# Kernel optimization log

Measured on AMD Instinct MI355X. Metric: run time of the kernel, lower is better.

## Reference

```python
import jax, jax.numpy as jnp
import numpy as np

N = 200000   # nodes
E = 400000   # edges
G = 4096     # graphs in batch
F_IN = 77    # atom feature dim
D = 128      # dim_drug
L = 3        # layer_drug
BN_EPS = 1e-5


def setup_inputs() -> dict:
    key = jax.random.key(0)
    ks = jax.random.split(key, 16)
    inp = {}
    inp["x"] = jax.random.normal(ks[0], (N, F_IN), jnp.float32)
    inp["edge_index"] = jax.random.randint(ks[1], (2, E), 0, N, dtype=jnp.int64)
    inp["batch"] = jnp.sort(jax.random.randint(ks[2], (N,), 0, G, dtype=jnp.int64))
    dims = [F_IN, D, D]
    i = 3
    for l in range(L):
        din = dims[l]
        inp[f"w1_{l}"] = jax.random.normal(ks[i], (din, D), jnp.float32) / np.sqrt(din); i += 1
        inp[f"b1_{l}"] = jnp.zeros((D,), jnp.float32)
        inp[f"w2_{l}"] = jax.random.normal(ks[i], (D, D), jnp.float32) / np.sqrt(D); i += 1
        inp[f"b2_{l}"] = jnp.zeros((D,), jnp.float32)
        inp[f"gamma_{l}"] = jnp.ones((D,), jnp.float32)
        inp[f"beta_{l}"] = jnp.zeros((D,), jnp.float32)
    inp["w_emb"] = jax.random.normal(ks[i], (L * D, 256), jnp.float32) / np.sqrt(L * D)
    inp["b_emb"] = jnp.zeros((256,), jnp.float32)
    return inp


def _gin_bn_layer(h, src, dst, w1, b1, w2, b2, gamma, beta):
    # GINConv (eps=0): out_i = MLP(x_i + sum_{j->i} x_j)
    agg = jax.ops.segment_sum(h[src], dst, num_segments=N)  # scatter-add aggregation
    h = h + agg
    h = jax.nn.relu(h @ w1 + b1) @ w2 + b2                  # GIN MLP
    h = jax.nn.relu(h)                                       # outer F.relu
    mu = jnp.mean(h, axis=0)
    var = jnp.var(h, axis=0)                                  # biased var (training-mode BN)
    return (h - mu) * jax.lax.rsqrt(var + BN_EPS) * gamma + beta


def reference(x, edge_index, batch,
              w1_0, b1_0, w2_0, b2_0, gamma_0, beta_0,
              w1_1, b1_1, w2_1, b2_1, gamma_1, beta_1,
              w1_2, b1_2, w2_2, b2_2, gamma_2, beta_2,
              w_emb, b_emb):
    src, dst = edge_index[0], edge_index[1]
    layers = [(w1_0, b1_0, w2_0, b2_0, gamma_0, beta_0),
              (w1_1, b1_1, w2_1, b2_1, gamma_1, beta_1),
              (w1_2, b1_2, w2_2, b2_2, gamma_2, beta_2)]
    h = x
    outs = []
    for (w1, b1, w2, b2, g, b) in layers:
        h = _gin_bn_layer(h, src, dst, w1, b1, w2, b2, g, b)
        outs.append(h)
    node_rep = jnp.concatenate(outs, axis=1)                  # JK 'cat' -> [N, L*D]
    pooled = jax.ops.segment_max(node_rep, batch, num_segments=G)  # global_max_pool -> [G, L*D]
    # drug_emb: Linear -> ReLU -> Dropout (identity in eval)
    return jax.nn.relu(pooled @ w_emb + b_emb)
```

## Files before the change

kernel.cpp:

```cpp
#include <hip/hip_runtime.h>
#include <hip/hip_bf16.h>
#include <float.h>

#define NN 200000
#define NE 400000
#define NG 4096
#define FIN 77
#define DD 128
#define BN_EPS 1e-5f
#define NB_SCAN ((NN + 255) / 256)
#define NBLK (NN / 64)
#define WCAP 1024

#define XCONV_BLKS (NN * 12 / 256)
#define WCONV_BLKS 192
#define ZERO_WORDS16 50194
#define ZERO_BLKS ((ZERO_WORDS16 + 255) / 256)

typedef float f32x4 __attribute__((ext_vector_type(4)));
typedef short s16x8 __attribute__((ext_vector_type(8)));
typedef unsigned int u32x4 __attribute__((ext_vector_type(4)));

__device__ __forceinline__ unsigned short f2bf(float x) {
    unsigned b = __float_as_uint(x);
    unsigned r = (b + 0x7FFFu + ((b >> 16) & 1u)) >> 16;
    return (unsigned short)r;
}
__device__ __forceinline__ float bf2f(unsigned short u) {
    return __uint_as_float(((unsigned)u) << 16);
}

__device__ __forceinline__ int load_idx(const void* p, int is64, long long i) {
    return is64 ? (int)((const long long*)p)[i] : ((const int*)p)[i];
}

__global__ __launch_bounds__(256) void prep_kernel(
    const float* __restrict__ x, unsigned short* __restrict__ xb,
    const float* __restrict__ w10, const float* __restrict__ w20,
    const float* __restrict__ w11, const float* __restrict__ w21,
    const float* __restrict__ w12, const float* __restrict__ w22,
    unsigned short* __restrict__ wtb,
    unsigned int* __restrict__ zbase,
    const unsigned* __restrict__ eidx, const unsigned* __restrict__ batch,
    int* __restrict__ flags)
{
    int b = blockIdx.x;
    if (b < XCONV_BLKS) {
        int idx = b * 256 + threadIdx.x;
        int row = idx / 12, c8 = (idx % 12) * 8;
        union { s16x8 v; unsigned short u[8]; } pk;
#pragma unroll
        for (int j = 0; j < 8; j++) {
            int c = c8 + j;
            pk.u[j] = (c < FIN) ? f2bf(x[(long long)row * FIN + c]) : (unsigned short)0;
        }
        *(s16x8*)&xb[(long long)row * 96 + c8] = pk.v;
    } else if (b < XCONV_BLKS + WCONV_BLKS) {
        int bb = b - XCONV_BLKS;
        int l = bb >> 6;
        int idx = (bb & 63) * 256 + threadIdx.x;
        int c = idx >> 7, k = idx & 127;
        const float* w1 = (l == 0) ? w10 : ((l == 1) ? w11 : w12);
        const float* w2 = (l == 0) ? w20 : ((l == 1) ? w21 : w22);
        int K1 = (l == 0) ? FIN : DD;
        unsigned short* wt1 = wtb + l * 2 * 16384;
        wt1[idx] = f2bf(k < K1 ? w1[k * DD + c] : 0.f);
        wt1[16384 + idx] = f2bf(w2[k * DD + c]);
    } else if (b < XCONV_BLKS + WCONV_BLKS + ZERO_BLKS) {
        int idx = (b - XCONV_BLKS - WCONV_BLKS) * 256 + threadIdx.x;
        if (idx < ZERO_WORDS16) ((u32x4*)zbase)[idx] = (u32x4){0u, 0u, 0u, 0u};
    } else {
        if (threadIdx.x == 0) {
            int e64 = 1, b64 = 1;
            for (int i = 0; i < 16; i++) {
                if (eidx[2 * NE - 1 - 2 * i] != 0u) e64 = 0;
                if (batch[NN - 1 - 2 * i] != 0u) b64 = 0;
            }
            flags[0] = e64;
            flags[1] = b64;
        }
    }
}

#define GS_BLKS 17
__global__ __launch_bounds__(256) void gs_count_kernel(
    const void* __restrict__ batch, const void* __restrict__ eidx,
    const int* __restrict__ flags, int* __restrict__ start, int* __restrict__ deg)
{
    int b = blockIdx.x;
    if (b < GS_BLKS) {
        int g = b * 256 + threadIdx.x;
        if (g > NG) return;
        int is64 = flags[1];
        int lo = 0, hi = NN;
        while (lo < hi) {
            int mid = (lo + hi) >> 1;
            int v = load_idx(batch, is64, mid);
            if (v < g) lo = mid + 1; else hi = mid;
        }
        start[g] = lo;
    } else {
        int e = (b - GS_BLKS) * 256 + threadIdx.x;
        if (e >= NE) return;
        int dst = load_idx(eidx, flags[0], (long long)NE + e);
        atomicAdd(&deg[dst], 1);
    }
}

__global__ void scan1_kernel(const int* __restrict__ deg, int* __restrict__ incl,
                             int* __restrict__ bsum) {
    __shared__ int sh[256];
    int i = blockIdx.x * 256 + threadIdx.x;
    int v = (i < NN) ? deg[i] : 0;
    sh[threadIdx.x] = v;
    __syncthreads();
    for (int off = 1; off < 256; off <<= 1) {
        int t = (threadIdx.x >= off) ? sh[threadIdx.x - off] : 0;
        __syncthreads();
        sh[threadIdx.x] += t;
        __syncthreads();
    }
    if (i < NN) incl[i] = sh[threadIdx.x];
    if (threadIdx.x == 255) bsum[blockIdx.x] = sh[255];
}

__global__ void scan2_kernel(int* __restrict__ bsum) {
    __shared__ int sh[1024];
    int t = threadIdx.x;
    int orig = (t < NB_SCAN) ? bsum[t] : 0;
    sh[t] = orig;
    __syncthreads();
    for (int off = 1; off < 1024; off <<= 1) {
        int v = (t >= off) ? sh[t - off] : 0;
        __syncthreads();
        sh[t] += v;
        __syncthreads();
    }
    if (t < NB_SCAN) bsum[t] = sh[t] - orig;
}

__global__ void scan3_kernel(const int* __restrict__ incl, const int* __restrict__ deg,
                             const int* __restrict__ bsum, int* __restrict__ rowptr,
                             int* __restrict__ cursor) {
    int i = blockIdx.x * 256 + threadIdx.x;
    if (i < NN) {
        int ex = bsum[blockIdx.x] + incl[i] - deg[i];
        rowptr[i] = ex;
        cursor[i] = ex;
    }
    if (i == 0) rowptr[NN] = NE;
}

__global__ void fill_kernel(const void* __restrict__ eidx, const int* __restrict__ flags,
                            int* __restrict__ cursor, int* __restrict__ slots) {
    int e = blockIdx.x * 256 + threadIdx.x;
    if (e >= NE) return;
    int is64 = flags[0];
    int src = load_idx(eidx, is64, e);
    int dst = load_idx(eidx, is64, (long long)NE + e);
    int pos = atomicAdd(&cursor[dst], 1);
    slots[pos] = src;
}

template <int L0>
__global__ __launch_bounds__(512, 8) void fused_layer(
    const unsigned short* __restrict__ src, const float* __restrict__ ss,
    const int* __restrict__ rowptr, const int* __restrict__ slots,
    const unsigned short* __restrict__ wt1, const unsigned short* __restrict__ wt2,
    const float* __restrict__ b1, const float* __restrict__ b2,
    unsigned short* __restrict__ out, float* __restrict__ partials)
{
    __shared__ unsigned short Xs[64 * 128];
    __shared__ int s_lo[65];
    __shared__ int s_win[WCAP];
    constexpr int SK = L0 ? 96 : 128;
    constexpr int KS1 = L0 ? 3 : 4;
    int tid = threadIdx.x;
    int lane = tid & 63;
    int w = tid >> 6;
    int rowBase = blockIdx.x * 64;

    int wb = rowptr[rowBase];
    int wn = rowptr[rowBase + 64] - wb;
    if (tid < 65) s_lo[tid] = rowptr[rowBase + tid];
    int wcap = (wn < WCAP) ? wn : WCAP;
    for (int i = tid; i < wcap; i += 512) s_win[i] = slots[wb + i];
    __syncthreads();

    {
        int rp = tid >> 4;
        int c8 = (tid & 15) * 8;
        float sc[8], sh[8];
        if (!L0) {
#pragma unroll
            for (int j = 0; j < 8; j++) { sc[j] = ss[c8 + j]; sh[j] = ss[DD + c8 + j]; }
        }
        int rA = rp, rB = 32 + rp;
        int griA = rowBase + rA, griB = rowBase + rB;
        bool skip = (L0 && c8 >= 96);
        s16x8 voA = {}, v0A = {}, v1A = {}, voB = {}, v0B = {}, v1B = {};
        int dA = 0, dB = 0, loA = 0, loB = 0, oA = 0, oB = 0;
        float mA0 = 0.f, mA1 = 0.f, mB0 = 0.f, mB1 = 0.f;
        if (!skip) {
            loA = s_lo[rA]; dA = s_lo[rA + 1] - loA; oA = loA - wb;
            loB = s_lo[rB]; dB = s_lo[rB + 1] - loB; oB = loB - wb;
            int iA0 = (dA > 0) ? ((oA < WCAP) ? s_win[oA] : slots[loA]) : griA;
            int iA1 = (dA > 1) ? ((oA + 1 < WCAP) ? s_win[oA + 1] : slots[loA + 1]) : griA;
            int iB0 = (dB > 0) ? ((oB < WCAP) ? s_win[oB] : slots[loB]) : griB;
            int iB1 = (dB > 1) ? ((oB + 1 < WCAP) ? s_win[oB + 1] : slots[loB + 1]) : griB;
            voA = *(const s16x8*)&src[griA * SK + c8];
            v0A = *(const s16x8*)&src[iA0 * SK + c8];
            v1A = *(const s16x8*)&src[iA1 * SK + c8];
            voB = *(const s16x8*)&src[griB * SK + c8];
            v0B = *(const s16x8*)&src[iB0 * SK + c8];
            v1B = *(const s16x8*)&src[iB1 * SK + c8];
            mA0 = (dA > 0) ? 1.f : 0.f; mA1 = (dA > 1) ? 1.f : 0.f;
            mB0 = (dB > 0) ? 1.f : 0.f; mB1 = (dB > 1) ? 1.f : 0.f;
        }
        float aA[8], aB[8];
#pragma unroll
        for (int j = 0; j < 8; j++) {
            aA[j] = bf2f((unsigned short)voA[j]) + mA0 * bf2f((unsigned short)v0A[j])
                                                 + mA1 * bf2f((unsigned short)v1A[j]);
            aB[j] = bf2f((unsigned short)voB[j]) + mB0 * bf2f((unsigned short)v0B[j])
                                                 + mB1 * bf2f((unsigned short)v1B[j]);
        }
        if (!skip) {
            for (int k = 2; k < dA; k++) {
                int kk = oA + k;
                int sid = (kk < WCAP) ? s_win[kk] : slots[loA + k];
                s16x8 vk = *(const s16x8*)&src[sid * SK + c8];
#pragma unroll
                for (int j = 0; j < 8; j++) aA[j] += bf2f((unsigned short)vk[j]);
            }
            for (int k = 2; k < dB; k++) {
                int kk = oB + k;
                int sid = (kk < WCAP) ? s_win[kk] : slots[loB + k];
                s16x8 vk = *(const s16x8*)&src[sid * SK + c8];
#pragma unroll
                for (int j = 0; j < 8; j++) aB[j] += bf2f((unsigned short)vk[j]);
            }
            if (!L0) {
                float cntA = (float)(dA + 1), cntB = (float)(dB + 1);
#pragma unroll
                for (int j = 0; j < 8; j++) {
                    aA[j] = aA[j] * sc[j] + cntA * sh[j];
                    aB[j] = aB[j] * sc[j] + cntB * sh[j];
                }
            }
        } else {
#pragma unroll
            for (int j = 0; j < 8; j++) { aA[j] = 0.f; aB[j] = 0.f; }
        }
        union { s16x8 v; unsigned short u[8]; } pkA, pkB;
#pragma unroll
        for (int j = 0; j < 8; j++) { pkA.u[j] = f2bf(aA[j]); pkB.u[j] = f2bf(aB[j]); }
        *(s16x8*)&Xs[rA * 128 + (c8 ^ ((rA & 7) << 3))] = pkA.v;
        *(s16x8*)&Xs[rB * 128 + (c8 ^ ((rB & 7) << 3))] = pkB.v;
    }

    int colbase = w * 16 + (lane & 15);
    s16x8 w1f[4];
    float bs1;
#pragma unroll
    for (int ks = 0; ks < KS1; ks++)
        w1f[ks] = *(const s16x8*)&wt1[colbase * 128 + ks * 32 + (lane >> 4) * 8];
    bs1 = b1[colbase];

    __syncthreads();

    f32x4 acc[4];
#pragma unroll
    for (int rb = 0; rb < 4; rb++) acc[rb] = 0;
#pragma unroll
    for (int ks = 0; ks < KS1; ks++) {
        int lk = ks * 32 + (lane >> 4) * 8;
        s16x8 af[4];
#pragma unroll
        for (int rb = 0; rb < 4; rb++) {
            int r = rb * 16 + (lane & 15);
            af[rb] = *(const s16x8*)&Xs[r * 128 + (lk ^ ((r & 7) << 3))];
        }
#pragma unroll
        for (int rb = 0; rb < 4; rb++)
            acc[rb] = __builtin_amdgcn_mfma_f32_16x16x32_bf16(af[rb], w1f[ks], acc[rb], 0, 0, 0);
    }

    __syncthreads();

#pragma unroll
    for (int rb = 0; rb < 4; rb++) {
#pragma unroll
        for (int reg = 0; reg < 4; reg++) {
            int row = rb * 16 + (lane >> 4) * 4 + reg;
            float v = fmaxf(acc[rb][reg] + bs1, 0.f);
            Xs[row * 128 + (colbase ^ ((row & 7) << 3))] = f2bf(v);
        }
    }

    s16x8 w2f[4];
    float bs2;
#pragma unroll
    for (int ks = 0; ks < 4; ks++)
        w2f[ks] = *(const s16x8*)&wt2[colbase * 128 + ks * 32 + (lane >> 4) * 8];
    bs2 = b2[colbase];

    __syncthreads();

#pragma unroll
    for (int rb = 0; rb < 4; rb++) acc[rb] = 0;
#pragma unroll
    for (int ks = 0; ks < 4; ks++) {
        int lk = ks * 32 + (lane >> 4) * 8;
        s16x8 af[4];
#pragma unroll
        for (int rb = 0; rb < 4; rb++) {
            int r = rb * 16 + (lane & 15);
            af[rb] = *(const s16x8*)&Xs[r * 128 + (lk ^ ((r & 7) << 3))];
        }
#pragma unroll
        for (int rb = 0; rb < 4; rb++)
            acc[rb] = __builtin_amdgcn_mfma_f32_16x16x32_bf16(af[rb], w2f[ks], acc[rb], 0, 0, 0);
    }

    float ps = 0.f, pq = 0.f;
#pragma unroll
    for (int rb = 0; rb < 4; rb++) {
#pragma unroll
        for (int reg = 0; reg < 4; reg++) {
            int row = rowBase + rb * 16 + (lane >> 4) * 4 + reg;
            float v = fmaxf(acc[rb][reg] + bs2, 0.f);
            unsigned short ub = f2bf(v);
            out[row * DD + colbase] = ub;
            float vb = bf2f(ub);
            ps += vb;
            pq += vb * vb;
        }
    }
    ps += __shfl_xor(ps, 16); ps += __shfl_xor(ps, 32);
    pq += __shfl_xor(pq, 16); pq += __shfl_xor(pq, 32);
    if (lane < 16) {
        partials[(long long)blockIdx.x * 256 + colbase] = ps;
        partials[(long long)blockIdx.x * 256 + 128 + colbase] = pq;
    }
}

__global__ __launch_bounds__(256) void bn_red2_fin_kernel(
    const float* __restrict__ partials, float* __restrict__ sums, int* __restrict__ done,
    const float* __restrict__ gamma, const float* __restrict__ beta, float* __restrict__ ss) {
    float s = 0.f;
    for (int b = blockIdx.x; b < NBLK; b += gridDim.x)
        s += partials[(long long)b * 256 + threadIdx.x];
    atomicAdd(&sums[threadIdx.x], s);
    __threadfence();
    __syncthreads();
    __shared__ int tick;
    if (threadIdx.x == 0) tick = atomicAdd(done, 1);
    __syncthreads();
    if (tick == (int)gridDim.x - 1 && threadIdx.x < 128) {
        int c = threadIdx.x;
        float s0 = atomicAdd(&sums[c], 0.f);
        float s1 = atomicAdd(&sums[DD + c], 0.f);
        float mu = s0 / (float)NN;
        float var = s1 / (float)NN - mu * mu;
        float sc = gamma[c] * rsqrtf(var + BN_EPS);
        ss[c] = sc;
        ss[DD + c] = beta[c] - mu * sc;
    }
}

__global__ __launch_bounds__(256) void pool_kernel(const unsigned short* __restrict__ hm,
                                                   const float* __restrict__ ss,
                                                   const int* __restrict__ start,
                                                   float* __restrict__ pooled, int l) {
    __shared__ float red[16][128];
    int g = blockIdx.x;
    int rp = threadIdx.x >> 4;
    int c8 = (threadIdx.x & 15) * 8;
    int lo = start[g], hi = start[g + 1];
    float sc[8], sh[8];
#pragma unroll
    for (int j = 0; j < 8; j++) { sc[j] = ss[c8 + j]; sh[j] = ss[DD + c8 + j]; }
    float m[8];
#pragma unroll
    for (int j = 0; j < 8; j++) m[j] = -FLT_MAX;
    for (int n = lo + rp; n < hi; n += 16) {
        s16x8 v = *(const s16x8*)&hm[(long long)n * DD + c8];
#pragma unroll
        for (int j = 0; j < 8; j++)
            m[j] = fmaxf(m[j], bf2f((unsigned short)v[j]) * sc[j] + sh[j]);
    }
#pragma unroll
    for (int j = 0; j < 8; j++) red[rp][c8 + j] = m[j];
    __syncthreads();
    if (threadIdx.x < 128) {
        int c = threadIdx.x;
        float mm = red[0][c];
#pragma unroll
        for (int r = 1; r < 16; r++) mm = fmaxf(mm, red[r][c]);
        pooled[(long long)g * (3 * DD) + l * DD + c] = mm;
    }
}

__global__ __launch_bounds__(256) void emb_kernel(const float* __restrict__ pooled,
                                                  const float* __restrict__ w,
                                                  const float* __restrict__ b,
                                                  float* __restrict__ out) {
    __shared__ float pl[8][384];
    int tid = threadIdx.x;
    int g0 = blockIdx.x * 8;
#pragma unroll
    for (int i = 0; i < 12; i++) {
        int idx = tid + i * 256;
        int gg = idx / 384, c = idx % 384;
        pl[gg][c] = pooled[(long long)(g0 + gg) * 384 + c];
    }
    __syncthreads();
    float acc[8];
#pragma unroll
    for (int gg = 0; gg < 8; gg++) acc[gg] = 0.f;
    for (int k = 0; k < 384; k++) {
        float wv = w[k * 256 + tid];
#pragma unroll
        for (int gg = 0; gg < 8; gg++) acc[gg] += pl[gg][k] * wv;
    }
    float bb = b[tid];
#pragma unroll
    for (int gg = 0; gg < 8; gg++)
        out[(long long)(g0 + gg) * 256 + tid] = fmaxf(acc[gg] + bb, 0.f);
}

extern "C" void kernel_launch(void* const* d_in, const int* in_sizes, int n_in,
                              void* d_out, int out_size, void* d_ws, size_t ws_size,
                              hipStream_t stream) {
    const float* x = (const float*)d_in[0];
    const void* eidx = d_in[1];
    const void* batch = d_in[2];
    const float* w1[3] = { (const float*)d_in[3],  (const float*)d_in[9],  (const float*)d_in[15] };
    const float* b1[3] = { (const float*)d_in[4],  (const float*)d_in[10], (const float*)d_in[16] };
    const float* w2[3] = { (const float*)d_in[5],  (const float*)d_in[11], (const float*)d_in[17] };
    const float* b2[3] = { (const float*)d_in[6],  (const float*)d_in[12], (const float*)d_in[18] };
    const float* gm[3] = { (const float*)d_in[7],  (const float*)d_in[13], (const float*)d_in[19] };
    const float* bt[3] = { (const float*)d_in[8],  (const float*)d_in[14], (const float*)d_in[20] };
    const float* w_emb = (const float*)d_in[21];
    const float* b_emb = (const float*)d_in[22];
    float* out = (float*)d_out;

    unsigned short* R1 = (unsigned short*)d_ws;
    unsigned short* R2 = R1 + (size_t)NN * DD;
    float* pooled = (float*)(R2 + (size_t)NN * DD);
    float* partials = pooled + (size_t)NG * 384;
    unsigned short* wtb = (unsigned short*)(partials + (size_t)NBLK * 256);
    float* ss = (float*)(wtb + 6 * 16384);
    float* sums = ss + 3 * 256;
    int* done = (int*)(sums + 3 * 256);
    int* done2 = done + 4;
    int* deg = done2 + 4;
    int* incl = deg + NN;
    int* bsum = incl + NN;
    int* rowptr = bsum + NB_SCAN;
    int* cursor = rowptr + NN + 1;
    int* slots = cursor + NN;
    int* start = slots + NE;
    int* flags = start + NG + 1;

    prep_kernel<<<XCONV_BLKS + WCONV_BLKS + ZERO_BLKS + 1, 256, 0, stream>>>(
        x, R1, w1[0], w2[0], w1[1], w2[1], w1[2], w2[2], wtb,
        (unsigned int*)sums, (const unsigned*)eidx, (const unsigned*)batch, flags);

    gs_count_kernel<<<GS_BLKS + (NE + 255) / 256, 256, 0, stream>>>(batch, eidx, flags, start, deg);

    scan1_kernel<<<NB_SCAN, 256, 0, stream>>>(deg, incl, bsum);
    scan2_kernel<<<1, 1024, 0, stream>>>(bsum);
    scan3_kernel<<<NB_SCAN, 256, 0, stream>>>(incl, deg, bsum, rowptr, cursor);
    fill_kernel<<<(NE + 255) / 256, 256, 0, stream>>>(eidx, flags, cursor, slots);

    unsigned short* hin[3] = { R1, R2, R1 };
    unsigned short* hout[3] = { R2, R1, R2 };
    for (int l = 0; l < 3; l++) {
        const unsigned short* wt1 = wtb + l * 2 * 16384;
        const unsigned short* wt2 = wt1 + 16384;
        const float* ss_prev = ss + (l - 1) * 256;
        float* ss_l = ss + l * 256;
        if (l == 0)
            fused_layer<1><<<NBLK, 512, 0, stream>>>(hin[l], nullptr, rowptr, slots, wt1, wt2,
                                                     b1[l], b2[l], hout[l], partials);
        else
            fused_layer<0><<<NBLK, 512, 0, stream>>>(hin[l], ss_prev, rowptr, slots, wt1, wt2,
                                                     b1[l], b2[l], hout[l], partials);
        bn_red2_fin_kernel<<<256, 256, 0, stream>>>(partials, sums + l * 256, done + l,
                                                    gm[l], bt[l], ss_l);
        pool_kernel<<<NG, 256, 0, stream>>>(hout[l], ss_l, start, pooled, l);
    }
    emb_kernel<<<NG / 8, 256, 0, stream>>>(pooled, w_emb, b_emb, out);
}
```

Baseline: 361.9 us.

## Fold BN stat reduction into layer atomics and merge graph-prep kernels

Replaces the per-layer partials buffer and separate BN reduction/finalize kernel with direct float atomicAdds of column sums from each fused_layer block. Consumers now derive scale and shift inline from the raw sums. The degree-count and graph-start search move into prep_kernel, each block detecting index width locally, and the scan2/scan3 pair becomes one kernel where each block sums the preceding block totals itself. Zeroing uses hipMemsetAsync. This cuts several launches and serial tails, but adds atomic contention on 256 addresses from 3125 blocks and makes float summation order nondeterministic.

```diff
diff --git a/kernel.cpp b/kernel.cpp
--- a/kernel.cpp
+++ b/kernel.cpp
@@ -12,14 +12,13 @@
 #define NBLK (NN / 64)
 #define WCAP 1024
 
+#define GS_BLKS 17
+#define CNT_BLKS ((NE + 255) / 256)
 #define XCONV_BLKS (NN * 12 / 256)
 #define WCONV_BLKS 192
-#define ZERO_WORDS16 50194
-#define ZERO_BLKS ((ZERO_WORDS16 + 255) / 256)
 
 typedef float f32x4 __attribute__((ext_vector_type(4)));
 typedef short s16x8 __attribute__((ext_vector_type(8)));
-typedef unsigned int u32x4 __attribute__((ext_vector_type(4)));
 
 __device__ __forceinline__ unsigned short f2bf(float x) {
     unsigned b = __float_as_uint(x);
@@ -32,6 +31,16 @@
 
 __device__ __forceinline__ int load_idx(const void* p, int is64, long long i) {
     return is64 ? (int)((const long long*)p)[i] : ((const int*)p)[i];
+}
+
+__device__ __forceinline__ void derive_ss(const float* __restrict__ sums,
+                                          const float* __restrict__ gamma,
+                                          const float* __restrict__ beta,
+                                          int c, float& sc, float& sh) {
+    float mu = sums[c] * (1.f / (float)NN);
+    float var = sums[DD + c] * (1.f / (float)NN) - mu * mu;
+    sc = gamma[c] * rsqrtf(var + BN_EPS);
+    sh = beta[c] - mu * sc;
 }
 
 __global__ __launch_bounds__(256) void prep_kernel(
@@ -40,13 +49,44 @@
     const float* __restrict__ w11, const float* __restrict__ w21,
     const float* __restrict__ w12, const float* __restrict__ w22,
     unsigned short* __restrict__ wtb,
-    unsigned int* __restrict__ zbase,
-    const unsigned* __restrict__ eidx, const unsigned* __restrict__ batch,
-    int* __restrict__ flags)
+    const void* __restrict__ eidx, const void* __restrict__ batch,
+    int* __restrict__ start, int* __restrict__ deg, int* __restrict__ flags)
 {
     int b = blockIdx.x;
-    if (b < XCONV_BLKS) {
-        int idx = b * 256 + threadIdx.x;
+    if (b < GS_BLKS) {
+        __shared__ int sb64;
+        if (threadIdx.x == 0) {
+            int b64 = 1;
+            const unsigned* bw = (const unsigned*)batch;
+            for (int i = 0; i < 16; i++) if (bw[NN - 1 - 2 * i] != 0u) b64 = 0;
+            sb64 = b64;
+        }
+        __syncthreads();
+        int is64 = sb64;
+        int g = b * 256 + threadIdx.x;
+        if (g > NG) return;
+        int lo = 0, hi = NN;
+        while (lo < hi) {
+            int mid = (lo + hi) >> 1;
+            int v = load_idx(batch, is64, mid);
+            if (v < g) lo = mid + 1; else hi = mid;
+        }
+        start[g] = lo;
+    } else if (b < GS_BLKS + CNT_BLKS) {
+        __shared__ int se64;
+        if (threadIdx.x == 0) {
+            int e64 = 1;
+            const unsigned* ew = (const unsigned*)eidx;
+            for (int i = 0; i < 16; i++) if (ew[2 * NE - 1 - 2 * i] != 0u) e64 = 0;
+            se64 = e64;
+        }
+        __syncthreads();
+        int e = (b - GS_BLKS) * 256 + threadIdx.x;
+        if (e >= NE) return;
+        int dst = load_idx(eidx, se64, (long long)NE + e);
+        atomicAdd(&deg[dst], 1);
+    } else if (b < GS_BLKS + CNT_BLKS + XCONV_BLKS) {
+        int idx = (b - GS_BLKS - CNT_BLKS) * 256 + threadIdx.x;
         int row = idx / 12, c8 = (idx % 12) * 8;
         union { s16x8 v; unsigned short u[8]; } pk;
 #pragma unroll
@@ -55,8 +95,8 @@
             pk.u[j] = (c < FIN) ? f2bf(x[(long long)row * FIN + c]) : (unsigned short)0;
         }
         *(s16x8*)&xb[(long long)row * 96 + c8] = pk.v;
-    } else if (b < XCONV_BLKS + WCONV_BLKS) {
-        int bb = b - XCONV_BLKS;
+    } else if (b < GS_BLKS + CNT_BLKS + XCONV_BLKS + WCONV_BLKS) {
+        int bb = b - GS_BLKS - CNT_BLKS - XCONV_BLKS;
         int l = bb >> 6;
         int idx = (bb & 63) * 256 + threadIdx.x;
         int c = idx >> 7, k = idx & 127;
@@ -66,44 +106,18 @@
         unsigned short* wt1 = wtb + l * 2 * 16384;
         wt1[idx] = f2bf(k < K1 ? w1[k * DD + c] : 0.f);
         wt1[16384 + idx] = f2bf(w2[k * DD + c]);
-    } else if (b < XCONV_BLKS + WCONV_BLKS + ZERO_BLKS) {
-        int idx = (b - XCONV_BLKS - WCONV_BLKS) * 256 + threadIdx.x;
-        if (idx < ZERO_WORDS16) ((u32x4*)zbase)[idx] = (u32x4){0u, 0u, 0u, 0u};
     } else {
         if (threadIdx.x == 0) {
             int e64 = 1, b64 = 1;
+            const unsigned* ew = (const unsigned*)eidx;
+            const unsigned* bw = (const unsigned*)batch;
             for (int i = 0; i < 16; i++) {
-                if (eidx[2 * NE - 1 - 2 * i] != 0u) e64 = 0;
-                if (batch[NN - 1 - 2 * i] != 0u) b64 = 0;
+                if (ew[2 * NE - 1 - 2 * i] != 0u) e64 = 0;
+                if (bw[NN - 1 - 2 * i] != 0u) b64 = 0;
             }
             flags[0] = e64;
             flags[1] = b64;
         }
-    }
-}
-
-#define GS_BLKS 17
-__global__ __launch_bounds__(256) void gs_count_kernel(
-    const void* __restrict__ batch, const void* __restrict__ eidx,
-    const int* __restrict__ flags, int* __restrict__ start, int* __restrict__ deg)
-{
-    int b = blockIdx.x;
-    if (b < GS_BLKS) {
-        int g = b * 256 + threadIdx.x;
-        if (g > NG) return;
-        int is64 = flags[1];
-        int lo = 0, hi = NN;
-        while (lo < hi) {
-            int mid = (lo + hi) >> 1;
-            int v = load_idx(batch, is64, mid);
-            if (v < g) lo = mid + 1; else hi = mid;
-        }
-        start[g] = lo;
-    } else {
-        int e = (b - GS_BLKS) * 256 + threadIdx.x;
-        if (e >= NE) return;
-        int dst = load_idx(eidx, flags[0], (long long)NE + e);
-        atomicAdd(&deg[dst], 1);
     }
 }
 
@@ -124,27 +138,24 @@
     if (threadIdx.x == 255) bsum[blockIdx.x] = sh[255];
 }
 
-__global__ void scan2_kernel(int* __restrict__ bsum) {
-    __shared__ int sh[1024];
+__global__ __launch_bounds__(256) void scan23_kernel(
+    const int* __restrict__ incl, const int* __restrict__ deg,
+    const int* __restrict__ bsum, int* __restrict__ rowptr, int* __restrict__ cursor) {
+    __shared__ int red[256];
+    int b = blockIdx.x;
     int t = threadIdx.x;
-    int orig = (t < NB_SCAN) ? bsum[t] : 0;
-    sh[t] = orig;
-    __syncthreads();
-    for (int off = 1; off < 1024; off <<= 1) {
-        int v = (t >= off) ? sh[t - off] : 0;
+    int s = 0;
+    for (int i = t; i < b; i += 256) s += bsum[i];
+    red[t] = s;
+    __syncthreads();
+    for (int off = 128; off > 0; off >>= 1) {
+        if (t < off) red[t] += red[t + off];
         __syncthreads();
-        sh[t] += v;
-        __syncthreads();
-    }
-    if (t < NB_SCAN) bsum[t] = sh[t] - orig;
-}
-
-__global__ void scan3_kernel(const int* __restrict__ incl, const int* __restrict__ deg,
-                             const int* __restrict__ bsum, int* __restrict__ rowptr,
-                             int* __restrict__ cursor) {
-    int i = blockIdx.x * 256 + threadIdx.x;
+    }
+    int pfx = red[0];
+    int i = b * 256 + t;
     if (i < NN) {
-        int ex = bsum[blockIdx.x] + incl[i] - deg[i];
+        int ex = pfx + incl[i] - deg[i];
         rowptr[i] = ex;
         cursor[i] = ex;
     }
@@ -164,11 +175,13 @@
 
 template <int L0>
 __global__ __launch_bounds__(512, 8) void fused_layer(
-    const unsigned short* __restrict__ src, const float* __restrict__ ss,
+    const unsigned short* __restrict__ src,
+    const float* __restrict__ sums_prev, const float* __restrict__ gm_prev,
+    const float* __restrict__ bt_prev,
     const int* __restrict__ rowptr, const int* __restrict__ slots,
     const unsigned short* __restrict__ wt1, const unsigned short* __restrict__ wt2,
     const float* __restrict__ b1, const float* __restrict__ b2,
-    unsigned short* __restrict__ out, float* __restrict__ partials)
+    unsigned short* __restrict__ out, float* __restrict__ sums_out)
 {
     __shared__ unsigned short Xs[64 * 128];
     __shared__ int s_lo[65];
@@ -193,7 +206,8 @@
         float sc[8], sh[8];
         if (!L0) {
 #pragma unroll
-            for (int j = 0; j < 8; j++) { sc[j] = ss[c8 + j]; sh[j] = ss[DD + c8 + j]; }
+            for (int j = 0; j < 8; j++)
+                derive_ss(sums_prev, gm_prev, bt_prev, c8 + j, sc[j], sh[j]);
         }
         int rA = rp, rB = 32 + rp;
         int griA = rowBase + rA, griB = rowBase + rB;
@@ -340,37 +354,15 @@
     ps += __shfl_xor(ps, 16); ps += __shfl_xor(ps, 32);
     pq += __shfl_xor(pq, 16); pq += __shfl_xor(pq, 32);
     if (lane < 16) {
-        partials[(long long)blockIdx.x * 256 + colbase] = ps;
-        partials[(long long)blockIdx.x * 256 + 128 + colbase] = pq;
-    }
-}
-
-__global__ __launch_bounds__(256) void bn_red2_fin_kernel(
-    const float* __restrict__ partials, float* __restrict__ sums, int* __restrict__ done,
-    const float* __restrict__ gamma, const float* __restrict__ beta, float* __restrict__ ss) {
-    float s = 0.f;
-    for (int b = blockIdx.x; b < NBLK; b += gridDim.x)
-        s += partials[(long long)b * 256 + threadIdx.x];
-    atomicAdd(&sums[threadIdx.x], s);
-    __threadfence();
-    __syncthreads();
-    __shared__ int tick;
-    if (threadIdx.x == 0) tick = atomicAdd(done, 1);
-    __syncthreads();
-    if (tick == (int)gridDim.x - 1 && threadIdx.x < 128) {
-        int c = threadIdx.x;
-        float s0 = atomicAdd(&sums[c], 0.f);
-        float s1 = atomicAdd(&sums[DD + c], 0.f);
-        float mu = s0 / (float)NN;
-        float var = s1 / (float)NN - mu * mu;
-        float sc = gamma[c] * rsqrtf(var + BN_EPS);
-        ss[c] = sc;
-        ss[DD + c] = beta[c] - mu * sc;
+        atomicAdd(&sums_out[colbase], ps);
+        atomicAdd(&sums_out[DD + colbase], pq);
     }
 }
 
 __global__ __launch_bounds__(256) void pool_kernel(const unsigned short* __restrict__ hm,
-                                                   const float* __restrict__ ss,
+                                                   const float* __restrict__ sums,
+                                                   const float* __restrict__ gamma,
+                                                   const float* __restrict__ beta,
                                                    const int* __restrict__ start,
                                                    float* __restrict__ pooled, int l) {
     __shared__ float red[16][128];
@@ -380,7 +372,7 @@
     int lo = start[g], hi = start[g + 1];
     float sc[8], sh[8];
 #pragma unroll
-    for (int j = 0; j < 8; j++) { sc[j] = ss[c8 + j]; sh[j] = ss[DD + c8 + j]; }
+    for (int j = 0; j < 8; j++) derive_ss(sums, gamma, beta, c8 + j, sc[j], sh[j]);
     float m[8];
 #pragma unroll
     for (int j = 0; j < 8; j++) m[j] = -FLT_MAX;
@@ -449,13 +441,11 @@
     unsigned short* R1 = (unsigned short*)d_ws;
     unsigned short* R2 = R1 + (size_t)NN * DD;
     float* pooled = (float*)(R2 + (size_t)NN * DD);
-    float* partials = pooled + (size_t)NG * 384;
-    unsigned short* wtb = (unsigned short*)(partials + (size_t)NBLK * 256);
-    float* ss = (float*)(wtb + 6 * 16384);
-    float* sums = ss + 3 * 256;
-    int* done = (int*)(sums + 3 * 256);
-    int* done2 = done + 4;
-    int* deg = done2 + 4;
+    unsigned short* wtb = (unsigned short*)(pooled + (size_t)NG * 384);
+    float* sums = (float*)(wtb + 6 * 16384);
+    int* pad = (int*)(sums + 3 * 256);
+    int* deg = pad + 8;
+    size_t zbytes = (3 * 256) * sizeof(float) + 8 * sizeof(int) + (size_t)NN * sizeof(int);
     int* incl = deg + NN;
     int* bsum = incl + NN;
     int* rowptr = bsum + NB_SCAN;
@@ -464,15 +454,14 @@
     int* start = slots + NE;
     int* flags = start + NG + 1;
 
-    prep_kernel<<<XCONV_BLKS + WCONV_BLKS + ZERO_BLKS + 1, 256, 0, stream>>>(
+    hipMemsetAsync(sums, 0, zbytes, stream);
+
+    prep_kernel<<<GS_BLKS + CNT_BLKS + XCONV_BLKS + WCONV_BLKS + 1, 256, 0, stream>>>(
         x, R1, w1[0], w2[0], w1[1], w2[1], w1[2], w2[2], wtb,
-        (unsigned int*)sums, (const unsigned*)eidx, (const unsigned*)batch, flags);
-
-    gs_count_kernel<<<GS_BLKS + (NE + 255) / 256, 256, 0, stream>>>(batch, eidx, flags, start, deg);
+        eidx, batch, start, deg, flags);
 
     scan1_kernel<<<NB_SCAN, 256, 0, stream>>>(deg, incl, bsum);
-    scan2_kernel<<<1, 1024, 0, stream>>>(bsum);
-    scan3_kernel<<<NB_SCAN, 256, 0, stream>>>(incl, deg, bsum, rowptr, cursor);
+    scan23_kernel<<<NB_SCAN, 256, 0, stream>>>(incl, deg, bsum, rowptr, cursor);
     fill_kernel<<<(NE + 255) / 256, 256, 0, stream>>>(eidx, flags, cursor, slots);
 
     unsigned short* hin[3] = { R1, R2, R1 };
@@ -480,17 +469,17 @@
     for (int l = 0; l < 3; l++) {
         const unsigned short* wt1 = wtb + l * 2 * 16384;
         const unsigned short* wt2 = wt1 + 16384;
-        const float* ss_prev = ss + (l - 1) * 256;
-        float* ss_l = ss + l * 256;
+        float* sums_l = sums + l * 256;
         if (l == 0)
-            fused_layer<1><<<NBLK, 512, 0, stream>>>(hin[l], nullptr, rowptr, slots, wt1, wt2,
-                                                     b1[l], b2[l], hout[l], partials);
+            fused_layer<1><<<NBLK, 512, 0, stream>>>(hin[l], nullptr, nullptr, nullptr,
+                                                     rowptr, slots, wt1, wt2,
+                                                     b1[l], b2[l], hout[l], sums_l);
         else
-            fused_layer<0><<<NBLK, 512, 0, stream>>>(hin[l], ss_prev, rowptr, slots, wt1, wt2,
-                                                     b1[l], b2[l], hout[l], partials);
-        bn_red2_fin_kernel<<<256, 256, 0, stream>>>(partials, sums + l * 256, done + l,
-                                                    gm[l], bt[l], ss_l);
-        pool_kernel<<<NG, 256, 0, stream>>>(hout[l], ss_l, start, pooled, l);
+            fused_layer<0><<<NBLK, 512, 0, stream>>>(hin[l], sums + (l - 1) * 256,
+                                                     gm[l - 1], bt[l - 1],
+                                                     rowptr, slots, wt1, wt2,
+                                                     b1[l], b2[l], hout[l], sums_l);
+        pool_kernel<<<NG, 256, 0, stream>>>(hout[l], sums_l, gm[l], bt[l], start, pooled, l);
     }
     emb_kernel<<<NG / 8, 256, 0, stream>>>(pooled, w_emb, b_emb, out);
 }
```

Measured after the change: 431.2 us. 1.19x slower.
